# Kernel optimization log

Measured on AMD Instinct MI355X. Metric: run time of the kernel, lower is better.

The kernel has to match this reference:

```python
import jax, jax.numpy as jnp
import numpy as np

HIDDEN = 2048
NUM_HEADS = 16
HEAD_DIM = HIDDEN // NUM_HEADS
ROPE_THETA = 10000.0


def _rope_cos_sin(n, dtype):
    # Llama-style: inv_freq over even indices, emb = concat([freqs, freqs])
    inv_freq = 1.0 / (ROPE_THETA ** (jnp.arange(0, HEAD_DIM, 2, dtype=jnp.float32) / HEAD_DIM))
    pos = jnp.arange(n, dtype=jnp.float32)
    freqs = pos[:, None] * inv_freq[None, :]          # [N, HEAD_DIM/2]
    emb = jnp.concatenate([freqs, freqs], axis=-1)    # [N, HEAD_DIM]
    return jnp.cos(emb).astype(dtype), jnp.sin(emb).astype(dtype)


def _rotate_half(x):
    x1, x2 = jnp.split(x, 2, axis=-1)
    return jnp.concatenate([-x2, x1], axis=-1)


def setup_inputs() -> dict:
    key = jax.random.key(0)
    ks = jax.random.split(key, 5)
    B, N, D = 2, 2048, HIDDEN
    s = 1.0 / np.sqrt(D)
    return {
        "x": jax.random.normal(ks[0], (B, N, D), jnp.float32),
        "Wq": jax.random.normal(ks[1], (D, D), jnp.float32) * s,
        "Wk": jax.random.normal(ks[2], (D, D), jnp.float32) * s,
        "Wv": jax.random.normal(ks[3], (D, D), jnp.float32) * s,
        "Wo": jax.random.normal(ks[4], (D, D), jnp.float32) * s,
    }


def reference(x, Wq, Wk, Wv, Wo):
    B, N, D = x.shape
    scale = HEAD_DIM ** -0.5

    def proj(W):  # nn.Linear(bias=False): x @ W.T, then split heads -> [B,H,N,hd]
        return (x @ W.T).reshape(B, N, NUM_HEADS, HEAD_DIM).transpose(0, 2, 1, 3)

    q, k, v = proj(Wq), proj(Wk), proj(Wv)

    cos, sin = _rope_cos_sin(N, x.dtype)  # [N, HEAD_DIM]
    cos = cos[None, None]                 # broadcast over B, H
    sin = sin[None, None]
    q = q * cos + _rotate_half(q) * sin
    k = k * cos + _rotate_half(k) * sin

    attn = jnp.einsum("bhqd,bhkd->bhqk", q, k) * scale  # full N x N scores
    attn = jax.nn.softmax(attn, axis=-1)                 # dropout p=0 -> identity
    out = jnp.einsum("bhqk,bhkd->bhqd", attn, v)
    out = out.transpose(0, 2, 1, 3).reshape(B, N, D)
    return out @ Wo.T
```

## Files before the change

### kernel.cpp

```cpp
#include <hip/hip_runtime.h>
#include <hip/hip_bf16.h>
#include <math.h>

typedef short bf16x8 __attribute__((ext_vector_type(8)));
typedef short bf16x4 __attribute__((ext_vector_type(4)));
typedef float f32x4 __attribute__((ext_vector_type(4)));

#define NSEQ 2048
#define DMODEL 2048
#define NH 16
#define HD 128
#define BATCH 2
#define MROWS 4096

__device__ __forceinline__ unsigned short f2b(float f) {
    __hip_bfloat16 h = __float2bfloat16(f);
    return *reinterpret_cast<unsigned short*>(&h);
}
__device__ __forceinline__ float b2f(unsigned short u) {
    __hip_bfloat16 h;
    *reinterpret_cast<unsigned short*>(&h) = u;
    return __bfloat162float(h);
}

__device__ __forceinline__ void gld_lds16(const unsigned short* g, unsigned short* l) {
    __builtin_amdgcn_global_load_lds(
        (const __attribute__((address_space(1))) unsigned int*)(const void*)g,
        (__attribute__((address_space(3))) unsigned int*)(void*)l,
        16, 0, 0);
}

__global__ __launch_bounds__(256) void cast_all_kernel(const float* __restrict__ x,
                                                       const float* __restrict__ wq,
                                                       const float* __restrict__ wk,
                                                       const float* __restrict__ wv,
                                                       const float* __restrict__ wo,
                                                       unsigned short* __restrict__ xb,
                                                       unsigned short* __restrict__ wqb) {
    int bid = blockIdx.x;
    const float* src;
    unsigned short* dst;
    int off;
    if (bid < 4096) {
        src = x; dst = xb; off = bid;
    } else {
        int w = (bid - 4096) >> 11;
        src = (w == 0) ? wq : (w == 1) ? wk : (w == 2) ? wv : wo;
        dst = wqb + (size_t)w * 4194304;
        off = (bid - 4096) & 2047;
    }
    int i = (off * 256 + threadIdx.x) * 8;
    float4 a = *(const float4*)(src + i);
    float4 b = *(const float4*)(src + i + 4);
    union { unsigned short u[8]; uint4 v; } tmp;
    tmp.u[0] = f2b(a.x); tmp.u[1] = f2b(a.y); tmp.u[2] = f2b(a.z); tmp.u[3] = f2b(a.w);
    tmp.u[4] = f2b(b.x); tmp.u[5] = f2b(b.y); tmp.u[6] = f2b(b.z); tmp.u[7] = f2b(b.w);
    *(uint4*)(dst + i) = tmp.v;
}

__global__ __launch_bounds__(256) void gemm_qkv(const unsigned short* __restrict__ A,
                                                const unsigned short* __restrict__ Bw,
                                                unsigned short* __restrict__ qk,
                                                unsigned short* __restrict__ vt) {
    __shared__ unsigned short sA[128 * 32];
    __shared__ unsigned short sB[128 * 32];
    const int K = DMODEL;
    const int tid = threadIdx.x;
    const int wave = tid >> 6, lane = tid & 63;
    const int m0 = blockIdx.y * 128, n0 = blockIdx.x * 128;
    const int wm = wave * 32;

    f32x4 acc[2][8] = {};

    const int srow = wave * 32 + (lane >> 2);
    const int scol = (lane & 3) * 8;
    const unsigned short* Ag = A + (size_t)(m0 + srow) * K + scol;
    const unsigned short* Bg = Bw + (size_t)(n0 + srow) * K + scol;
    unsigned short* sA0 = &sA[(wave * 32) * 32];
    unsigned short* sA1 = &sA[(wave * 32 + 16) * 32];
    unsigned short* sB0 = &sB[(wave * 32) * 32];
    unsigned short* sB1 = &sB[(wave * 32 + 16) * 32];
    const int fr = lane & 15, fo = (lane >> 4) * 8;

    for (int kb = 0; kb < K; kb += 32) {
        gld_lds16(Ag + kb, sA0);
        gld_lds16(Ag + (size_t)16 * K + kb, sA1);
        gld_lds16(Bg + kb, sB0);
        gld_lds16(Bg + (size_t)16 * K + kb, sB1);
        __syncthreads();
        bf16x8 af[2], bfr[8];
        #pragma unroll
        for (int mt = 0; mt < 2; mt++)
            af[mt] = *(const bf16x8*)&sA[(wm + mt * 16 + fr) * 32 + fo];
        #pragma unroll
        for (int nt = 0; nt < 8; nt++)
            bfr[nt] = *(const bf16x8*)&sB[(nt * 16 + fr) * 32 + fo];
        #pragma unroll
        for (int mt = 0; mt < 2; mt++)
            #pragma unroll
            for (int nt = 0; nt < 8; nt++)
                acc[mt][nt] = __builtin_amdgcn_mfma_f32_16x16x32_bf16(af[mt], bfr[nt], acc[mt][nt], 0, 0, 0);
        __syncthreads();
    }

    const int g4 = (lane >> 4) * 4, c0 = lane & 15;
    if (n0 < 4096) {
        const float scale = (n0 < 2048) ? 0.08838834764831845f : 1.0f;
        unsigned short* dst = qk + (size_t)(n0 >> 11) * 8388608;
        const int colbase = n0 & 2047;
        float invf[4];
        #pragma unroll
        for (int nt = 0; nt < 4; nt++)
            invf[nt] = exp2f((float)(nt * 16 + c0) * -0.2076205059304545f);
        #pragma unroll
        for (int mt = 0; mt < 2; mt++) {
            #pragma unroll
            for (int r = 0; r < 4; r++) {
                int row = m0 + wm + mt * 16 + g4 + r;
                float nf = (float)(row & (NSEQ - 1));
                size_t rbase = (size_t)row * 2048 + colbase + c0;
                #pragma unroll
                for (int nt = 0; nt < 4; nt++) {
                    float sv, cv;
                    __sincosf(nf * invf[nt], &sv, &cv);
                    float lo = acc[mt][nt][r], hi = acc[mt][nt + 4][r];
                    dst[rbase + nt * 16]      = f2b((lo * cv - hi * sv) * scale);
                    dst[rbase + nt * 16 + 64] = f2b((hi * cv + lo * sv) * scale);
                }
            }
        }
    } else {
        #pragma unroll
        for (int mt = 0; mt < 2; mt++) {
            int mbase = m0 + wm + mt * 16 + g4;
            int bb = mbase >> 11;
            int nn = mbase & 2047;
            #pragma unroll
            for (int nt = 0; nt < 8; nt++) {
                int d = n0 - 4096 + nt * 16 + c0;
                union { unsigned short u[4]; uint2 v; } o;
                #pragma unroll
                for (int r = 0; r < 4; r++) o.u[r] = f2b(acc[mt][nt][r]);
                *(uint2*)(vt + ((size_t)(bb * 2048 + d)) * 2048 + nn) = o.v;
            }
        }
    }
}

__global__ __launch_bounds__(256) void gemm_out(const unsigned short* __restrict__ A,
                                                const unsigned short* __restrict__ Bw,
                                                float* __restrict__ Cf) {
    __shared__ unsigned short sA[128 * 64];
    __shared__ unsigned short sB[128 * 64];
    const int K = DMODEL, Nn = DMODEL;
    const int tid = threadIdx.x;
    const int wave = tid >> 6, lane = tid & 63;
    const int m0 = blockIdx.y * 128, n0 = blockIdx.x * 128;
    const int wm = (wave >> 1) * 64, wn = (wave & 1) * 64;

    f32x4 acc[4][4] = {};

    const int srowoff = wave * 8 + (lane >> 3);
    const int gchunk = ((lane & 7) ^ ((lane >> 3) & 7)) * 8;
    const unsigned short* Ag = A + (size_t)(m0 + srowoff) * K + gchunk;
    const unsigned short* Bg = Bw + (size_t)(n0 + srowoff) * K + gchunk;
    unsigned short* sAw = &sA[(wave * 8) * 64];
    unsigned short* sBw = &sB[(wave * 8) * 64];

    const int fr = lane & 15, grp = lane >> 4;
    const int swz = fr & 7;

    for (int kb = 0; kb < K; kb += 64) {
        #pragma unroll
        for (int i = 0; i < 4; i++)
            gld_lds16(Ag + (size_t)(i * 32) * K + kb, sAw + i * 32 * 64);
        #pragma unroll
        for (int i = 0; i < 4; i++)
            gld_lds16(Bg + (size_t)(i * 32) * K + kb, sBw + i * 32 * 64);
        __syncthreads();
        #pragma unroll
        for (int ks = 0; ks < 2; ks++) {
            bf16x8 af[4], bfr[4];
            #pragma unroll
            for (int mt = 0; mt < 4; mt++)
                af[mt] = *(const bf16x8*)&sA[(wm + mt * 16 + fr) * 64 + (((ks * 4 + grp) ^ swz) << 3)];
            #pragma unroll
            for (int nt = 0; nt < 4; nt++)
                bfr[nt] = *(const bf16x8*)&sB[(wn + nt * 16 + fr) * 64 + (((ks * 4 + grp) ^ swz) << 3)];
            #pragma unroll
            for (int mt = 0; mt < 4; mt++)
                #pragma unroll
                for (int nt = 0; nt < 4; nt++)
                    acc[mt][nt] = __builtin_amdgcn_mfma_f32_16x16x32_bf16(af[mt], bfr[nt], acc[mt][nt], 0, 0, 0);
        }
        __syncthreads();
    }

    const int g4 = (lane >> 4) * 4, c0 = lane & 15;
    #pragma unroll
    for (int mt = 0; mt < 4; mt++)
        #pragma unroll
        for (int nt = 0; nt < 4; nt++) {
            int col = n0 + wn + nt * 16 + c0;
            #pragma unroll
            for (int r = 0; r < 4; r++) {
                int row = m0 + wm + mt * 16 + g4 + r;
                Cf[(size_t)row * Nn + col] = acc[mt][nt][r];
            }
        }
}

__global__ __launch_bounds__(256) void attn_kernel(const unsigned short* __restrict__ Q,
                                                   const unsigned short* __restrict__ Kg,
                                                   const unsigned short* __restrict__ Vt,
                                                   unsigned short* __restrict__ O) {
    __shared__ unsigned short sK[2][64 * 128];
    __shared__ unsigned short sV[2][128 * 64];

    const int lin = blockIdx.x;
    const int swz = (lin & 7) * 64 + (lin >> 3);
    const int qt = swz & 15;
    const int bh = swz >> 4;
    const int b = bh >> 4, h = bh & 15;
    const int tid = threadIdx.x, wave = tid >> 6, lane = tid & 63;
    const int c0 = lane & 15, grp = lane >> 4;

    bf16x8 qf[2][4];
    {
        const unsigned short* Qbase = Q + (size_t)(b * NSEQ + qt * 128 + wave * 32 + c0) * DMODEL + h * HD + grp * 8;
        #pragma unroll
        for (int nt = 0; nt < 2; nt++)
            #pragma unroll
            for (int ks = 0; ks < 4; ks++)
                qf[nt][ks] = *(const bf16x8*)(Qbase + (size_t)nt * 16 * DMODEL + ks * 32);
    }

    f32x4 oacc[8][2] = {};
    float lsum[2] = {0.f, 0.f};

    const unsigned short* Kbase = Kg + (size_t)(b * NSEQ) * DMODEL + h * HD;
    const unsigned short* Vbase = Vt + (size_t)(bh * HD) * NSEQ;

    #define ATTN_STAGE(bi, kv0)                                                        \
        {                                                                              \
            _Pragma("unroll")                                                          \
            for (int i = 0; i < 4; i++) {                                              \
                int rr = wave * 16 + i * 4 + (lane >> 4);                              \
                int gc = ((lane & 15) ^ (rr & 15)) * 8;                                \
                gld_lds16(Kbase + (size_t)((kv0) + rr) * DMODEL + gc,                  \
                          &sK[bi][(wave * 16 + i * 4) * 128]);                         \
            }                                                                          \
            _Pragma("unroll")                                                          \
            for (int i = 0; i < 4; i++) {                                              \
                int rr = wave * 32 + i * 8 + (lane >> 3);                              \
                int gc = ((lane & 7) ^ (lane >> 3)) * 8;                               \
                gld_lds16(Vbase + (size_t)rr * NSEQ + (kv0) + gc,                      \
                          &sV[bi][(wave * 32 + i * 8) * 64]);                          \
            }                                                                          \
        }

    ATTN_STAGE(0, 0);
    __syncthreads();

    for (int it = 0; it < 32; it++) {
        const unsigned short* sKb = sK[it & 1];
        const unsigned short* sVb = sV[it & 1];

        if (it < 31) {
            ATTN_STAGE((it + 1) & 1, (it + 1) * 64);
        }
        __builtin_amdgcn_sched_barrier(0);

        f32x4 s[4][2] = {};
        #pragma unroll
        for (int ks = 0; ks < 4; ks++) {
            bf16x8 kf[4];
            #pragma unroll
            for (int mt = 0; mt < 4; mt++)
                kf[mt] = *(const bf16x8*)&sKb[(mt * 16 + c0) * 128 + (((ks * 4 + grp) ^ c0) << 3)];
            #pragma unroll
            for (int mt = 0; mt < 4; mt++)
                #pragma unroll
                for (int nt = 0; nt < 2; nt++)
                    s[mt][nt] = __builtin_amdgcn_mfma_f32_16x16x32_bf16(kf[mt], qf[nt][ks], s[mt][nt], 0, 0, 0);
        }

        bf16x4 pk[4][2];
        #pragma unroll
        for (int mt = 0; mt < 4; mt++)
            #pragma unroll
            for (int nt = 0; nt < 2; nt++) {
                float p0 = __expf(s[mt][nt][0]);
                float p1 = __expf(s[mt][nt][1]);
                float p2 = __expf(s[mt][nt][2]);
                float p3 = __expf(s[mt][nt][3]);
                lsum[nt] += (p0 + p1) + (p2 + p3);
                bf16x4 t;
                t[0] = (short)f2b(p0); t[1] = (short)f2b(p1);
                t[2] = (short)f2b(p2); t[3] = (short)f2b(p3);
                pk[mt][nt] = t;
            }

        #pragma unroll
        for (int mtK = 0; mtK < 4; mtK++) {
            bf16x4 va[8];
            #pragma unroll
            for (int mo = 0; mo < 8; mo++)
                va[mo] = *(const bf16x4*)&sVb[(mo * 16 + c0) * 64
                                              + (((mtK * 2 + (grp >> 1)) ^ (c0 & 7)) << 3)
                                              + (grp & 1) * 4];
            #pragma unroll
            for (int mo = 0; mo < 8; mo++)
                #pragma unroll
                for (int nt = 0; nt < 2; nt++)
                    oacc[mo][nt] = __builtin_amdgcn_mfma_f32_16x16x16bf16_1k(va[mo], pk[mtK][nt], oacc[mo][nt], 0, 0, 0);
        }

        __syncthreads();
    }

    float invl[2];
    #pragma unroll
    for (int nt = 0; nt < 2; nt++) {
        float li = lsum[nt];
        li += __shfl_xor(li, 16);
        li += __shfl_xor(li, 32);
        invl[nt] = 1.0f / li;
    }
    #pragma unroll
    for (int mo = 0; mo < 8; mo++)
        #pragma unroll
        for (int nt = 0; nt < 2; nt++) {
            union { unsigned short u[4]; uint2 v; } o;
            #pragma unroll
            for (int r = 0; r < 4; r++)
                o.u[r] = f2b(oacc[mo][nt][r] * invl[nt]);
            int row = b * NSEQ + qt * 128 + wave * 32 + nt * 16 + c0;
            int col = h * HD + mo * 16 + grp * 4;
            *(uint2*)(O + (size_t)row * DMODEL + col) = o.v;
        }
}

extern "C" void kernel_launch(void* const* d_in, const int* in_sizes, int n_in,
                              void* d_out, int out_size, void* d_ws, size_t ws_size,
                              hipStream_t stream) {
    const float* x  = (const float*)d_in[0];
    const float* Wq = (const float*)d_in[1];
    const float* Wk = (const float*)d_in[2];
    const float* Wv = (const float*)d_in[3];
    const float* Wo = (const float*)d_in[4];

    char* ws = (char*)d_ws;
    unsigned short* xb  = (unsigned short*)(ws);
    unsigned short* wqb = (unsigned short*)(ws + 16777216);
    unsigned short* wob = (unsigned short*)(ws + 16777216 + 3 * 8388608);
    unsigned short* qb  = (unsigned short*)(ws + 50331648);
    unsigned short* kb  = (unsigned short*)(ws + 67108864);
    unsigned short* vt  = (unsigned short*)(ws + 83886080);

    cast_all_kernel<<<12288, 256, 0, stream>>>(x, Wq, Wk, Wv, Wo, xb, wqb);

    gemm_qkv<<<dim3(48, 32), 256, 0, stream>>>(xb, wqb, qb, vt);

    attn_kernel<<<512, 256, 0, stream>>>(qb, kb, vt, xb);

    gemm_out<<<dim3(16, 32), 256, 0, stream>>>(xb, wob, (float*)d_out);
}
```

Baseline: 380.8 us.

## Restructure QKV GEMM with 128x384 tiles, 4-stage async LDS pipeline, XCD mapping

Rewrites the QKV projection GEMM to use 512-thread blocks computing 128x384 tiles. Global-to-LDS loads run through a 4-slot ring buffer with explicit vmcnt waits in place of two syncthreads per k-step. The change also adds an XOR swizzle on the LDS layout, MFMA priority raising, and a block-to-XCD mapping so blocks sharing weight columns land on the same die. The RoPE/V-transpose epilogue is remapped so each 384-wide tile spans Q/K/V region boundaries, which adds per-column branching and larger register and LDS usage (96KB LDS).

```diff
diff --git a/kernel.cpp b/kernel.cpp
--- a/kernel.cpp
+++ b/kernel.cpp
@@ -58,90 +58,126 @@
     *(uint4*)(dst + i) = tmp.v;
 }
 
-__global__ __launch_bounds__(256) void gemm_qkv(const unsigned short* __restrict__ A,
-                                                const unsigned short* __restrict__ Bw,
-                                                unsigned short* __restrict__ qk,
-                                                unsigned short* __restrict__ vt) {
-    __shared__ unsigned short sA[128 * 32];
-    __shared__ unsigned short sB[128 * 32];
+__global__ __launch_bounds__(512, 2) void gemm_qkv(const unsigned short* __restrict__ A,
+                                                   const unsigned short* __restrict__ Bw,
+                                                   unsigned short* __restrict__ qk,
+                                                   unsigned short* __restrict__ vt) {
+    __shared__ unsigned short sA[4][128 * 32];
+    __shared__ unsigned short sB[4][384 * 32];
     const int K = DMODEL;
     const int tid = threadIdx.x;
     const int wave = tid >> 6, lane = tid & 63;
-    const int m0 = blockIdx.y * 128, n0 = blockIdx.x * 128;
-    const int wm = wave * 32;
-
-    f32x4 acc[2][8] = {};
-
-    const int srow = wave * 32 + (lane >> 2);
-    const int scol = (lane & 3) * 8;
-    const unsigned short* Ag = A + (size_t)(m0 + srow) * K + scol;
-    const unsigned short* Bg = Bw + (size_t)(n0 + srow) * K + scol;
-    unsigned short* sA0 = &sA[(wave * 32) * 32];
-    unsigned short* sA1 = &sA[(wave * 32 + 16) * 32];
-    unsigned short* sB0 = &sB[(wave * 32) * 32];
-    unsigned short* sB1 = &sB[(wave * 32 + 16) * 32];
-    const int fr = lane & 15, fo = (lane >> 4) * 8;
-
-    for (int kb = 0; kb < K; kb += 32) {
-        gld_lds16(Ag + kb, sA0);
-        gld_lds16(Ag + (size_t)16 * K + kb, sA1);
-        gld_lds16(Bg + kb, sB0);
-        gld_lds16(Bg + (size_t)16 * K + kb, sB1);
-        __syncthreads();
-        bf16x8 af[2], bfr[8];
-        #pragma unroll
-        for (int mt = 0; mt < 2; mt++)
-            af[mt] = *(const bf16x8*)&sA[(wm + mt * 16 + fr) * 32 + fo];
-        #pragma unroll
-        for (int nt = 0; nt < 8; nt++)
-            bfr[nt] = *(const bf16x8*)&sB[(nt * 16 + fr) * 32 + fo];
-        #pragma unroll
-        for (int mt = 0; mt < 2; mt++)
-            #pragma unroll
-            for (int nt = 0; nt < 8; nt++)
+
+    const int bid = blockIdx.x;
+    const int xcd = bid & 7, cc_ = bid >> 3;
+    const int m0 = (cc_ & 31) * 128;
+    const int n0 = (xcd * 2 + (cc_ >> 5)) * 384;
+
+    const int wr = wave >> 2, wc = wave & 3;
+    const int fr = lane & 15, grp = lane >> 4;
+    const int rsw = (grp ^ ((fr >> 1) & 3)) << 3;
+
+    const int sr = wave * 16 + (lane >> 2);
+    const int sc = (((lane & 3) ^ ((lane >> 3) & 3)) << 3);
+    const unsigned short* Ag = A + (size_t)(m0 + sr) * K + sc;
+    const unsigned short* Bg = Bw + (size_t)(n0 + sr) * K + sc;
+
+    f32x4 acc[4][6] = {};
+
+    #define QKV_STAGE(sl, t)                                                          \
+        {                                                                             \
+            gld_lds16(Ag + (t) * 32, &sA[sl][(wave * 16) * 32]);                      \
+            gld_lds16(Bg + (t) * 32, &sB[sl][(wave * 16) * 32]);                      \
+            gld_lds16(Bg + (size_t)128 * K + (t) * 32, &sB[sl][(128 + wave * 16) * 32]); \
+            gld_lds16(Bg + (size_t)256 * K + (t) * 32, &sB[sl][(256 + wave * 16) * 32]); \
+        }
+
+    QKV_STAGE(0, 0);
+    QKV_STAGE(1, 1);
+    QKV_STAGE(2, 2);
+    __builtin_amdgcn_sched_barrier(0);
+    asm volatile("s_waitcnt vmcnt(8)" ::: "memory");
+    asm volatile("s_barrier" ::: "memory");
+
+    const int aoff = (wr * 64 + fr) * 32 + rsw;
+    const int boff = (wc * 16 + fr) * 32 + rsw;
+
+    for (int s = 0; s < 64; s++) {
+        const int slot = s & 3;
+        if (s < 61) { QKV_STAGE((s + 3) & 3, s + 3); }
+
+        bf16x8 af[4], bfr[6];
+        #pragma unroll
+        for (int mt = 0; mt < 4; mt++)
+            af[mt] = *(const bf16x8*)&sA[slot][aoff + mt * 512];
+        #pragma unroll
+        for (int nt = 0; nt < 6; nt++)
+            bfr[nt] = *(const bf16x8*)&sB[slot][boff + nt * 2048];
+
+        __builtin_amdgcn_sched_barrier(0);
+        asm volatile("s_waitcnt lgkmcnt(0)" ::: "memory");
+        __builtin_amdgcn_sched_barrier(0);
+        __builtin_amdgcn_s_setprio(1);
+        #pragma unroll
+        for (int mt = 0; mt < 4; mt++)
+            #pragma unroll
+            for (int nt = 0; nt < 6; nt++)
                 acc[mt][nt] = __builtin_amdgcn_mfma_f32_16x16x32_bf16(af[mt], bfr[nt], acc[mt][nt], 0, 0, 0);
-        __syncthreads();
-    }
-
-    const int g4 = (lane >> 4) * 4, c0 = lane & 15;
+        __builtin_amdgcn_s_setprio(0);
+        __builtin_amdgcn_sched_barrier(0);
+        if (s < 61)       { asm volatile("s_waitcnt vmcnt(8)" ::: "memory"); }
+        else if (s == 61) { asm volatile("s_waitcnt vmcnt(4)" ::: "memory"); }
+        else if (s == 62) { asm volatile("s_waitcnt vmcnt(0)" ::: "memory"); }
+        asm volatile("s_barrier" ::: "memory");
+    }
+    #undef QKV_STAGE
+
+    const int g4 = grp * 4, c0 = fr;
+    const int colb = n0 + wc * 16 + c0;
     if (n0 < 4096) {
-        const float scale = (n0 < 2048) ? 0.08838834764831845f : 1.0f;
-        unsigned short* dst = qk + (size_t)(n0 >> 11) * 8388608;
-        const int colbase = n0 & 2047;
-        float invf[4];
-        #pragma unroll
-        for (int nt = 0; nt < 4; nt++)
-            invf[nt] = exp2f((float)(nt * 16 + c0) * -0.2076205059304545f);
-        #pragma unroll
-        for (int mt = 0; mt < 2; mt++) {
+        const float inv = exp2f((float)(wc * 16 + c0) * -0.2076205059304545f);
+        #pragma unroll
+        for (int mt = 0; mt < 4; mt++) {
             #pragma unroll
             for (int r = 0; r < 4; r++) {
-                int row = m0 + wm + mt * 16 + g4 + r;
+                int row = m0 + wr * 64 + mt * 16 + g4 + r;
                 float nf = (float)(row & (NSEQ - 1));
-                size_t rbase = (size_t)row * 2048 + colbase + c0;
+                float sv, cv;
+                __sincosf(nf * inv, &sv, &cv);
+                size_t rb = (size_t)row * 2048;
                 #pragma unroll
-                for (int nt = 0; nt < 4; nt++) {
-                    float sv, cv;
-                    __sincosf(nf * invf[nt], &sv, &cv);
-                    float lo = acc[mt][nt][r], hi = acc[mt][nt + 4][r];
-                    dst[rbase + nt * 16]      = f2b((lo * cv - hi * sv) * scale);
-                    dst[rbase + nt * 16 + 64] = f2b((hi * cv + lo * sv) * scale);
+                for (int p = 0; p < 3; p++) {
+                    int collo = colb + p * 128;
+                    if (collo < 4096) {
+                        int region = collo >> 11;
+                        float scale = (region == 0) ? 0.08838834764831845f : 1.0f;
+                        unsigned short* dst = qk + (size_t)region * 8388608 + (collo & 2047);
+                        float lo = acc[mt][2 * p][r], hi = acc[mt][2 * p + 1][r];
+                        dst[rb]      = f2b((lo * cv - hi * sv) * scale);
+                        dst[rb + 64] = f2b((hi * cv + lo * sv) * scale);
+                    }
                 }
             }
         }
-    } else {
-        #pragma unroll
-        for (int mt = 0; mt < 2; mt++) {
-            int mbase = m0 + wm + mt * 16 + g4;
-            int bb = mbase >> 11;
-            int nn = mbase & 2047;
-            #pragma unroll
-            for (int nt = 0; nt < 8; nt++) {
-                int d = n0 - 4096 + nt * 16 + c0;
-                union { unsigned short u[4]; uint2 v; } o;
+    }
+    if (n0 + 383 >= 4096) {
+        #pragma unroll
+        for (int p = 0; p < 3; p++) {
+            int collo = colb + p * 128;
+            if (collo >= 4096) {
                 #pragma unroll
-                for (int r = 0; r < 4; r++) o.u[r] = f2b(acc[mt][nt][r]);
-                *(uint2*)(vt + ((size_t)(bb * 2048 + d)) * 2048 + nn) = o.v;
+                for (int j = 0; j < 2; j++) {
+                    int d = collo + j * 64 - 4096;
+                    #pragma unroll
+                    for (int mt = 0; mt < 4; mt++) {
+                        int row0 = m0 + wr * 64 + mt * 16 + g4;
+                        int bb = row0 >> 11, nn = row0 & 2047;
+                        union { unsigned short u[4]; uint2 v; } o;
+                        #pragma unroll
+                        for (int r = 0; r < 4; r++) o.u[r] = f2b(acc[mt][2 * p + j][r]);
+                        *(uint2*)(vt + ((size_t)(bb * 2048 + d)) * 2048 + nn) = o.v;
+                    }
+                }
             }
         }
     }
@@ -318,6 +354,7 @@
 
         __syncthreads();
     }
+    #undef ATTN_STAGE
 
     float invl[2];
     #pragma unroll
@@ -360,7 +397,7 @@
 
     cast_all_kernel<<<12288, 256, 0, stream>>>(x, Wq, Wk, Wv, Wo, xb, wqb);
 
-    gemm_qkv<<<dim3(48, 32), 256, 0, stream>>>(xb, wqb, qb, vt);
+    gemm_qkv<<<512, 512, 0, stream>>>(xb, wqb, qb, vt);
 
     attn_kernel<<<512, 256, 0, stream>>>(qb, kb, vt, xb);
 
```

New measurement: 407.8 us. 7.1% more time.

## Halve attention tile sizes to double grid and raise occupancy

Applied to the files above, without the earlier changes.

Shrinks the attention block to 64 query rows with one 16-row tile per wave, and the KV step to 32 keys with retuned LDS swizzles. Doubles the launch grid and adds a launch bound of 4 blocks per CU to cut register and LDS pressure and hide latency. The cost is more global K/V traffic per query, twice as many loop iterations and barriers, and less MFMA work between syncs.

```diff
diff --git a/kernel.cpp b/kernel.cpp
--- a/kernel.cpp
+++ b/kernel.cpp
@@ -210,33 +210,31 @@
         }
 }
 
-__global__ __launch_bounds__(256) void attn_kernel(const unsigned short* __restrict__ Q,
-                                                   const unsigned short* __restrict__ Kg,
-                                                   const unsigned short* __restrict__ Vt,
-                                                   unsigned short* __restrict__ O) {
-    __shared__ unsigned short sK[2][64 * 128];
-    __shared__ unsigned short sV[2][128 * 64];
+__global__ __launch_bounds__(256, 4) void attn_kernel(const unsigned short* __restrict__ Q,
+                                                      const unsigned short* __restrict__ Kg,
+                                                      const unsigned short* __restrict__ Vt,
+                                                      unsigned short* __restrict__ O) {
+    __shared__ unsigned short sK[2][32 * 128];
+    __shared__ unsigned short sV[2][128 * 32];
 
     const int lin = blockIdx.x;
-    const int swz = (lin & 7) * 64 + (lin >> 3);
-    const int qt = swz & 15;
-    const int bh = swz >> 4;
+    const int swz = (lin & 7) * 128 + (lin >> 3);
+    const int qt = swz & 31;
+    const int bh = swz >> 5;
     const int b = bh >> 4, h = bh & 15;
     const int tid = threadIdx.x, wave = tid >> 6, lane = tid & 63;
     const int c0 = lane & 15, grp = lane >> 4;
 
-    bf16x8 qf[2][4];
+    bf16x8 qf[4];
     {
-        const unsigned short* Qbase = Q + (size_t)(b * NSEQ + qt * 128 + wave * 32 + c0) * DMODEL + h * HD + grp * 8;
-        #pragma unroll
-        for (int nt = 0; nt < 2; nt++)
-            #pragma unroll
-            for (int ks = 0; ks < 4; ks++)
-                qf[nt][ks] = *(const bf16x8*)(Qbase + (size_t)nt * 16 * DMODEL + ks * 32);
-    }
-
-    f32x4 oacc[8][2] = {};
-    float lsum[2] = {0.f, 0.f};
+        const unsigned short* Qbase = Q + (size_t)(b * NSEQ + qt * 64 + wave * 16 + c0) * DMODEL + h * HD + grp * 8;
+        #pragma unroll
+        for (int ks = 0; ks < 4; ks++)
+            qf[ks] = *(const bf16x8*)(Qbase + ks * 32);
+    }
+
+    f32x4 oacc[8] = {};
+    float lsum = 0.f;
 
     const unsigned short* Kbase = Kg + (size_t)(b * NSEQ) * DMODEL + h * HD;
     const unsigned short* Vbase = Vt + (size_t)(bh * HD) * NSEQ;
@@ -244,101 +242,91 @@
     #define ATTN_STAGE(bi, kv0)                                                        \
         {                                                                              \
             _Pragma("unroll")                                                          \
-            for (int i = 0; i < 4; i++) {                                              \
-                int rr = wave * 16 + i * 4 + (lane >> 4);                              \
+            for (int j = 0; j < 2; j++) {                                              \
+                int rr = j * 16 + wave * 4 + (lane >> 4);                              \
                 int gc = ((lane & 15) ^ (rr & 15)) * 8;                                \
                 gld_lds16(Kbase + (size_t)((kv0) + rr) * DMODEL + gc,                  \
-                          &sK[bi][(wave * 16 + i * 4) * 128]);                         \
+                          &sK[bi][(j * 16 + wave * 4) * 128]);                         \
             }                                                                          \
             _Pragma("unroll")                                                          \
-            for (int i = 0; i < 4; i++) {                                              \
-                int rr = wave * 32 + i * 8 + (lane >> 3);                              \
-                int gc = ((lane & 7) ^ (lane >> 3)) * 8;                               \
+            for (int j = 0; j < 2; j++) {                                              \
+                int rr = j * 64 + wave * 16 + (lane >> 2);                             \
+                int gc = ((lane & 3) ^ ((rr >> 1) & 3)) * 8;                           \
                 gld_lds16(Vbase + (size_t)rr * NSEQ + (kv0) + gc,                      \
-                          &sV[bi][(wave * 32 + i * 8) * 64]);                          \
+                          &sV[bi][(j * 64 + wave * 16) * 32]);                         \
             }                                                                          \
         }
 
     ATTN_STAGE(0, 0);
     __syncthreads();
 
-    for (int it = 0; it < 32; it++) {
+    for (int it = 0; it < 64; it++) {
         const unsigned short* sKb = sK[it & 1];
         const unsigned short* sVb = sV[it & 1];
 
-        if (it < 31) {
-            ATTN_STAGE((it + 1) & 1, (it + 1) * 64);
+        if (it < 63) {
+            ATTN_STAGE((it + 1) & 1, (it + 1) * 32);
         }
         __builtin_amdgcn_sched_barrier(0);
 
-        f32x4 s[4][2] = {};
+        f32x4 s[2] = {};
         #pragma unroll
         for (int ks = 0; ks < 4; ks++) {
-            bf16x8 kf[4];
-            #pragma unroll
-            for (int mt = 0; mt < 4; mt++)
+            bf16x8 kf[2];
+            #pragma unroll
+            for (int mt = 0; mt < 2; mt++)
                 kf[mt] = *(const bf16x8*)&sKb[(mt * 16 + c0) * 128 + (((ks * 4 + grp) ^ c0) << 3)];
             #pragma unroll
-            for (int mt = 0; mt < 4; mt++)
-                #pragma unroll
-                for (int nt = 0; nt < 2; nt++)
-                    s[mt][nt] = __builtin_amdgcn_mfma_f32_16x16x32_bf16(kf[mt], qf[nt][ks], s[mt][nt], 0, 0, 0);
-        }
-
-        bf16x4 pk[4][2];
-        #pragma unroll
-        for (int mt = 0; mt < 4; mt++)
-            #pragma unroll
-            for (int nt = 0; nt < 2; nt++) {
-                float p0 = __expf(s[mt][nt][0]);
-                float p1 = __expf(s[mt][nt][1]);
-                float p2 = __expf(s[mt][nt][2]);
-                float p3 = __expf(s[mt][nt][3]);
-                lsum[nt] += (p0 + p1) + (p2 + p3);
-                bf16x4 t;
-                t[0] = (short)f2b(p0); t[1] = (short)f2b(p1);
-                t[2] = (short)f2b(p2); t[3] = (short)f2b(p3);
-                pk[mt][nt] = t;
-            }
-
-        #pragma unroll
-        for (int mtK = 0; mtK < 4; mtK++) {
+            for (int mt = 0; mt < 2; mt++)
+                s[mt] = __builtin_amdgcn_mfma_f32_16x16x32_bf16(kf[mt], qf[ks], s[mt], 0, 0, 0);
+        }
+
+        bf16x4 pk[2];
+        #pragma unroll
+        for (int mt = 0; mt < 2; mt++) {
+            float p0 = __expf(s[mt][0]);
+            float p1 = __expf(s[mt][1]);
+            float p2 = __expf(s[mt][2]);
+            float p3 = __expf(s[mt][3]);
+            lsum += (p0 + p1) + (p2 + p3);
+            bf16x4 t;
+            t[0] = (short)f2b(p0); t[1] = (short)f2b(p1);
+            t[2] = (short)f2b(p2); t[3] = (short)f2b(p3);
+            pk[mt] = t;
+        }
+
+        #pragma unroll
+        for (int mtK = 0; mtK < 2; mtK++) {
             bf16x4 va[8];
             #pragma unroll
             for (int mo = 0; mo < 8; mo++)
-                va[mo] = *(const bf16x4*)&sVb[(mo * 16 + c0) * 64
-                                              + (((mtK * 2 + (grp >> 1)) ^ (c0 & 7)) << 3)
+                va[mo] = *(const bf16x4*)&sVb[(mo * 16 + c0) * 32
+                                              + (((mtK * 2 + (grp >> 1)) ^ ((c0 >> 1) & 3)) << 3)
                                               + (grp & 1) * 4];
             #pragma unroll
             for (int mo = 0; mo < 8; mo++)
-                #pragma unroll
-                for (int nt = 0; nt < 2; nt++)
-                    oacc[mo][nt] = __builtin_amdgcn_mfma_f32_16x16x16bf16_1k(va[mo], pk[mtK][nt], oacc[mo][nt], 0, 0, 0);
-        }
-
-        __syncthreads();
-    }
-
-    float invl[2];
+                oacc[mo] = __builtin_amdgcn_mfma_f32_16x16x16bf16_1k(va[mo], pk[mtK], oacc[mo], 0, 0, 0);
+        }
+
+        __syncthreads();
+    }
+    #undef ATTN_STAGE
+
+    float li = lsum;
+    li += __shfl_xor(li, 16);
+    li += __shfl_xor(li, 32);
+    const float invl = 1.0f / li;
+
     #pragma unroll
-    for (int nt = 0; nt < 2; nt++) {
-        float li = lsum[nt];
-        li += __shfl_xor(li, 16);
-        li += __shfl_xor(li, 32);
-        invl[nt] = 1.0f / li;
-    }
-    #pragma unroll
-    for (int mo = 0; mo < 8; mo++)
-        #pragma unroll
-        for (int nt = 0; nt < 2; nt++) {
-            union { unsigned short u[4]; uint2 v; } o;
-            #pragma unroll
-            for (int r = 0; r < 4; r++)
-                o.u[r] = f2b(oacc[mo][nt][r] * invl[nt]);
-            int row = b * NSEQ + qt * 128 + wave * 32 + nt * 16 + c0;
-            int col = h * HD + mo * 16 + grp * 4;
-            *(uint2*)(O + (size_t)row * DMODEL + col) = o.v;
-        }
+    for (int mo = 0; mo < 8; mo++) {
+        union { unsigned short u[4]; uint2 v; } o;
+        #pragma unroll
+        for (int r = 0; r < 4; r++)
+            o.u[r] = f2b(oacc[mo][r] * invl);
+        int row = b * NSEQ + qt * 64 + wave * 16 + c0;
+        int col = h * HD + mo * 16 + grp * 4;
+        *(uint2*)(O + (size_t)row * DMODEL + col) = o.v;
+    }
 }
 
 extern "C" void kernel_launch(void* const* d_in, const int* in_sizes, int n_in,
@@ -362,7 +350,7 @@
 
     gemm_qkv<<<dim3(48, 32), 256, 0, stream>>>(xb, wqb, qb, vt);
 
-    attn_kernel<<<512, 256, 0, stream>>>(qb, kb, vt, xb);
+    attn_kernel<<<1024, 256, 0, stream>>>(qb, kb, vt, xb);
 
     gemm_out<<<dim3(16, 32), 256, 0, stream>>>(xb, wob, (float*)d_out);
 }
```

After: 397.3 us. 4.3% more time.
